# Performance work log

Hardware: AMD Instinct MI355X
Metric: run time of the kernel (lower is better)

The kernel has to match this reference:

```python
import jax, jax.numpy as jnp
import numpy as np

ALPHA = 1000.0  # softmin temperature from the original module


def setup_inputs() -> dict:
    key = jax.random.key(0)
    ks = jax.random.split(key, 10)
    B, D, H, E, K = 8192, 784, 256, 32, 512
    s = 0.05  # small init scale to keep activations/distances numerically sane
    return {
        "x": jax.random.normal(ks[0], (B, D), jnp.float32),
        "cluster_reps": jax.random.normal(ks[1], (K, E), jnp.float32),
        "W1": jax.random.normal(ks[2], (D, H), jnp.float32) * s,
        "b1": jnp.zeros((H,), jnp.float32),
        "W2": jax.random.normal(ks[3], (H, E), jnp.float32) * s,
        "b2": jnp.zeros((E,), jnp.float32),
        "W3": jax.random.normal(ks[4], (E, H), jnp.float32) * s,
        "b3": jnp.zeros((H,), jnp.float32),
        "W4": jax.random.normal(ks[5], (H, D), jnp.float32) * s,
        "b4": jnp.zeros((D,), jnp.float32),
    }


def reference(x, cluster_reps, W1, b1, W2, b2, W3, b3, W4, b4):
    # --- autoencoder: 2-layer MLP encoder / decoder ---
    h = jax.nn.relu(x @ W1 + b1)            # [B, H]
    embeddings = h @ W2 + b2                # [B, E]
    h2 = jax.nn.relu(embeddings @ W3 + b3)  # [B, H]
    reconstruction = h2 @ W4 + b4           # [B, D]

    # --- squared distances to cluster reps: [B, K] ---
    diff = embeddings[:, None, :] - cluster_reps[None, :, :]  # [B, K, E]
    distances = jnp.sum(diff * diff, axis=2)                  # [B, K]

    # --- stable softmin-weighted distances ---
    min_dist = jnp.min(distances, axis=1, keepdims=True)       # [B, 1]
    exponentials = jnp.exp(-ALPHA * (distances - min_dist))    # [B, K]
    sum_exponentials = jnp.sum(exponentials, axis=1, keepdims=True)
    weighted_dists = distances * (exponentials / sum_exponentials)

    return (weighted_dists, distances, reconstruction, embeddings)
```

## Files before the change

### kernel.cpp

```cpp
#include <hip/hip_runtime.h>
#include <cstddef>

#define NB 8192
#define ND 784
#define NH 256
#define NE 32
#define NK 512
#define ALPHA_F 1000.0f

typedef _Float16 h8 __attribute__((ext_vector_type(8)));
typedef float f32x4 __attribute__((ext_vector_type(4)));

__global__ __launch_bounds__(256)
void splitw2_kernel(const float* __restrict__ W1, _Float16* __restrict__ w1thi,
                    _Float16* __restrict__ w1tlo,
                    const float* __restrict__ W4, _Float16* __restrict__ w4thi,
                    _Float16* __restrict__ w4tlo) {
    const int b = blockIdx.x;
    const float* W; _Float16 *hi, *lo; int K, N, n;
    if (b < NH) { W = W1; hi = w1thi; lo = w1tlo; K = ND; N = NH; n = b; }
    else        { W = W4; hi = w4thi; lo = w4tlo; K = NH; N = ND; n = b - NH; }
    for (int k = threadIdx.x; k < K; k += 256) {
        float w = W[(size_t)k * N + n];
        _Float16 hh = (_Float16)w;
        float r = w - (float)hh;
        hi[(size_t)n * K + k] = hh;
        lo[(size_t)n * K + k] = (_Float16)(r * 2048.0f);
    }
}

template<int TERMS, bool RELU, bool SPLITA, int MT>
__device__ __forceinline__ void gemm_body(
    const float* __restrict__ Af32,
    const _Float16* __restrict__ Ahi_g,
    const _Float16* __restrict__ Alo_g,
    const _Float16* __restrict__ WThi,
    const _Float16* __restrict__ WTlo,
    const float* __restrict__ bias, float* __restrict__ C,
    int N, int K, int KS, int bx, int by, int tid,
    _Float16* __restrict__ sAhi, _Float16* __restrict__ sAlo,
    _Float16* __restrict__ sBhi, _Float16* __restrict__ sBlo) {
    constexpr int BM  = MT * 32;
    constexpr int ACH = BM / 64;
    constexpr int AS  = BM * 40;
    constexpr int BS  = 64 * 40;

    const int bm = bx * BM;
    const int bn = by * 64;

    const int arow = (ACH == 1) ? (tid >> 2) : (tid >> 1);
    const int ak   = (ACH == 1) ? ((tid & 3) * 8) : ((tid & 1) * 16);
    const int brow = tid >> 2;
    const int bk   = (tid & 3) * 8;

    const float*    pA32 = SPLITA ? Af32 + (size_t)(bm + arow) * K : nullptr;
    const _Float16* pAhi = SPLITA ? nullptr : Ahi_g + (size_t)(bm + arow) * K;
    const _Float16* pAlo = SPLITA ? nullptr : Alo_g + (size_t)(bm + arow) * K;
    int brow_g = bn + brow; if (brow_g > N - 1) brow_g = N - 1;
    const _Float16* pBhi = WThi + (size_t)brow_g * K;
    const _Float16* pBlo = WTlo + (size_t)brow_g * K;

    float araw[ACH * 8];
    h8 rahi[ACH], ralo[ACH];
    h8 rbhi, rblo;

    auto prefetch = [&](int s) {
        #pragma unroll
        for (int c = 0; c < ACH; ++c) {
            const int k = s * 32 + ak + c * 8;
            if (SPLITA) {
                if (k + 8 <= K) {
                    f32x4 v0 = *(const f32x4*)(pA32 + k);
                    f32x4 v1 = *(const f32x4*)(pA32 + k + 4);
                    #pragma unroll
                    for (int j = 0; j < 4; ++j) {
                        araw[c * 8 + j]     = v0[j];
                        araw[c * 8 + 4 + j] = v1[j];
                    }
                } else {
                    #pragma unroll
                    for (int j = 0; j < 8; ++j) araw[c * 8 + j] = 0.f;
                }
            } else {
                rahi[c] = (k + 8 <= K) ? *(const h8*)(pAhi + k) : (h8){};
                ralo[c] = (k + 8 <= K) ? *(const h8*)(pAlo + k) : (h8){};
            }
        }
        const int kb = s * 32 + bk;
        rbhi = (kb + 8 <= K) ? *(const h8*)(pBhi + kb) : (h8){};
        rblo = (kb + 8 <= K) ? *(const h8*)(pBlo + kb) : (h8){};
    };

    auto commit = [&](int buf) {
        #pragma unroll
        for (int c = 0; c < ACH; ++c) {
            h8 hi, lo;
            if (SPLITA) {
                #pragma unroll
                for (int j = 0; j < 8; ++j) {
                    float v = araw[c * 8 + j];
                    _Float16 hh = (_Float16)v;
                    hi[j] = hh;
                    lo[j] = (_Float16)((v - (float)hh) * 2048.0f);
                }
            } else { hi = rahi[c]; lo = ralo[c]; }
            *(h8*)&sAhi[buf * AS + arow * 40 + ak + c * 8] = hi;
            *(h8*)&sAlo[buf * AS + arow * 40 + ak + c * 8] = lo;
        }
        *(h8*)&sBhi[buf * BS + brow * 40 + bk] = rbhi;
        *(h8*)&sBlo[buf * BS + brow * 40 + bk] = rblo;
    };

    prefetch(0);
    commit(0);
    prefetch(1);
    __syncthreads();

    const int lane = tid & 63;
    const int wv   = tid >> 6;
    const int wm   = (wv >> 1) * (MT * 16);
    const int wn   = (wv & 1) * 32;
    const int li   = lane & 15;
    const int kq   = (lane >> 4) * 8;

    f32x4 acc0[MT][2] = {};
    f32x4 acc1[MT][2] = {};
    f32x4 acc2[MT][2] = {};

    for (int s = 0; s < KS; ++s) {
        const int buf = s & 1;
        h8 fahi[MT], falo[MT], fbhi[2], fblo[2];
        #pragma unroll
        for (int mt = 0; mt < MT; ++mt) {
            const int ao = buf * AS + (wm + mt * 16 + li) * 40 + kq;
            fahi[mt] = *(const h8*)&sAhi[ao];
            falo[mt] = *(const h8*)&sAlo[ao];
        }
        #pragma unroll
        for (int nt = 0; nt < 2; ++nt) {
            const int bo = buf * BS + (wn + nt * 16 + li) * 40 + kq;
            fbhi[nt] = *(const h8*)&sBhi[bo];
            fblo[nt] = *(const h8*)&sBlo[bo];
        }
        #pragma unroll
        for (int mt = 0; mt < MT; ++mt)
            #pragma unroll
            for (int nt = 0; nt < 2; ++nt) {
                acc0[mt][nt] = __builtin_amdgcn_mfma_f32_16x16x32_f16(
                    fahi[mt], fbhi[nt], acc0[mt][nt], 0, 0, 0);
                acc1[mt][nt] = __builtin_amdgcn_mfma_f32_16x16x32_f16(
                    fahi[mt], fblo[nt], acc1[mt][nt], 0, 0, 0);
                acc1[mt][nt] = __builtin_amdgcn_mfma_f32_16x16x32_f16(
                    falo[mt], fbhi[nt], acc1[mt][nt], 0, 0, 0);
                if (TERMS == 4)
                    acc2[mt][nt] = __builtin_amdgcn_mfma_f32_16x16x32_f16(
                        falo[mt], fblo[nt], acc2[mt][nt], 0, 0, 0);
            }
        if (s + 1 < KS) {
            commit((s + 1) & 1);
            if (s + 2 < KS) prefetch(s + 2);
        }
        __syncthreads();
    }

    const float c1 = 1.0f / 2048.0f;
    const float c2 = c1 * c1;
    const int quad = lane >> 4;
    #pragma unroll
    for (int nt = 0; nt < 2; ++nt) {
        const int n = bn + wn + nt * 16 + li;
        if (n < N) {
            const float bv = bias[n];
            #pragma unroll
            for (int mt = 0; mt < MT; ++mt) {
                #pragma unroll
                for (int r = 0; r < 4; ++r) {
                    const int m = bm + wm + mt * 16 + quad * 4 + r;
                    float v = acc0[mt][nt][r] + c1 * acc1[mt][nt][r];
                    if (TERMS == 4) v += c2 * acc2[mt][nt][r];
                    v += bv;
                    if (RELU) v = fmaxf(v, 0.f);
                    C[(size_t)m * N + n] = v;
                }
            }
        }
    }
}

template<int TERMS, bool RELU, bool SPLITA, int MT>
__global__ __launch_bounds__(256)
void mfma_gemm3(const float* __restrict__ Af32,
                const _Float16* __restrict__ Ahi_g,
                const _Float16* __restrict__ Alo_g,
                const _Float16* __restrict__ WThi,
                const _Float16* __restrict__ WTlo,
                const float* __restrict__ bias, float* __restrict__ C,
                int N, int K, int KS) {
    constexpr int BM = MT * 32;
    __shared__ __align__(16) _Float16 smem[2 * BM * 40 * 2 + 2 * 64 * 40 * 2];
    _Float16* sAhi = smem;
    _Float16* sAlo = sAhi + 2 * BM * 40;
    _Float16* sBhi = sAlo + 2 * BM * 40;
    _Float16* sBlo = sBhi + 2 * 64 * 40;
    gemm_body<TERMS, RELU, SPLITA, MT>(Af32, Ahi_g, Alo_g, WThi, WTlo, bias, C,
                                       N, K, KS, blockIdx.x, blockIdx.y,
                                       threadIdx.x, sAhi, sAlo, sBhi, sBlo);
}

__global__ __launch_bounds__(256)
void mid_kernel(const float* __restrict__ h, const float* __restrict__ W2,
                const float* __restrict__ b2, const float* __restrict__ W3,
                const float* __restrict__ b3, float* __restrict__ emb,
                _Float16* __restrict__ h2hi, _Float16* __restrict__ h2lo) {
    __shared__ float es[16][32];
    const int tid = threadIdx.x;
    const int r0  = blockIdx.x * 16;

    #pragma unroll
    for (int half = 0; half < 2; ++half) {
        const int o   = tid + half * 256;
        const int row = o >> 5;
        const int col = o & 31;
        const float* hrow = h + (size_t)(r0 + row) * NH;
        float acc0 = 0.f, acc1 = 0.f;
        #pragma unroll 4
        for (int k = 0; k < NH; k += 4) {
            float4 hv = *(const float4*)(hrow + k);
            acc0 = fmaf(hv.x, W2[(k + 0) * NE + col], acc0);
            acc1 = fmaf(hv.y, W2[(k + 1) * NE + col], acc1);
            acc0 = fmaf(hv.z, W2[(k + 2) * NE + col], acc0);
            acc1 = fmaf(hv.w, W2[(k + 3) * NE + col], acc1);
        }
        float v = acc0 + acc1 + b2[col];
        es[row][col] = v;
        emb[(size_t)r0 * NE + o] = v;
    }
    __syncthreads();

    const int col = tid;
    float acc[16];
    #pragma unroll
    for (int r = 0; r < 16; ++r) acc[r] = 0.f;
    #pragma unroll
    for (int k = 0; k < NE; ++k) {
        float w = W3[k * NH + col];
        #pragma unroll
        for (int r = 0; r < 16; ++r) acc[r] = fmaf(es[r][k], w, acc[r]);
    }
    const float bb = b3[col];
    #pragma unroll
    for (int r = 0; r < 16; ++r) {
        float v = acc[r] + bb;
        v = v > 0.f ? v : 0.f;
        _Float16 hh = (_Float16)v;
        float rr = v - (float)hh;
        h2hi[(size_t)(r0 + r) * NH + col] = hh;
        h2lo[(size_t)(r0 + r) * NH + col] = (_Float16)(rr * 2048.0f);
    }
}

__device__ __forceinline__ void dist_body256(
    const float* __restrict__ emb, const float* __restrict__ reps,
    float* __restrict__ dist, float* __restrict__ wout,
    int blk, int tid, float* __restrict__ es, float* __restrict__ tr,
    float* __restrict__ rmin, float* __restrict__ rinv) {
    const int r0 = blk * 8;
    es[tid] = emb[(size_t)r0 * NE + tid];

    const float* rp0 = reps + (size_t)tid * NE;
    const float* rp1 = reps + (size_t)(tid + 256) * NE;
    f32x4 rv0[8], rv1[8];
    #pragma unroll
    for (int e4 = 0; e4 < 8; ++e4) {
        rv0[e4] = ((const f32x4*)rp0)[e4];
        rv1[e4] = ((const f32x4*)rp1)[e4];
    }
    __syncthreads();

    float d0[8], d1[8];
    #pragma unroll
    for (int r = 0; r < 8; ++r) {
        float a0 = 0.f, a1 = 0.f;
        #pragma unroll
        for (int e4 = 0; e4 < 8; ++e4) {
            f32x4 ev = *(const f32x4*)&es[r * 32 + e4 * 4];
            #pragma unroll
            for (int j = 0; j < 4; ++j) {
                float t0 = ev[j] - rv0[e4][j];
                a0 = fmaf(t0, t0, a0);
                float t1 = ev[j] - rv1[e4][j];
                a1 = fmaf(t1, t1, a1);
            }
        }
        d0[r] = a0; d1[r] = a1;
    }

    const int lane = tid & 63;
    const int wv   = tid >> 6;

    #pragma unroll
    for (int r = 0; r < 8; ++r) {
        tr[r * 520 + tid]       = d0[r];
        tr[r * 520 + 256 + tid] = d1[r];
    }
    __syncthreads();
    #pragma unroll
    for (int p = 0; p < 2; ++p) {
        const int rr = wv + p * 4;
        f32x4 a = *(const f32x4*)&tr[rr * 520 + lane * 8];
        f32x4 b = *(const f32x4*)&tr[rr * 520 + lane * 8 + 4];
        float m = fminf(fminf(fminf(a[0], a[1]), fminf(a[2], a[3])),
                        fminf(fminf(b[0], b[1]), fminf(b[2], b[3])));
        #pragma unroll
        for (int off = 32; off > 0; off >>= 1)
            m = fminf(m, __shfl_xor(m, off, 64));
        if (lane == 0) rmin[rr] = m;
    }
    __syncthreads();

    float e0[8], e1[8];
    #pragma unroll
    for (int r = 0; r < 8; ++r) {
        e0[r] = expf(-ALPHA_F * (d0[r] - rmin[r]));
        e1[r] = expf(-ALPHA_F * (d1[r] - rmin[r]));
        tr[r * 520 + tid]       = e0[r];
        tr[r * 520 + 256 + tid] = e1[r];
    }
    __syncthreads();
    #pragma unroll
    for (int p = 0; p < 2; ++p) {
        const int rr = wv + p * 4;
        f32x4 a = *(const f32x4*)&tr[rr * 520 + lane * 8];
        f32x4 b = *(const f32x4*)&tr[rr * 520 + lane * 8 + 4];
        float s = ((a[0] + a[1]) + (a[2] + a[3])) +
                  ((b[0] + b[1]) + (b[2] + b[3]));
        #pragma unroll
        for (int off = 32; off > 0; off >>= 1)
            s += __shfl_xor(s, off, 64);
        if (lane == 0) rinv[rr] = 1.0f / s;
    }
    __syncthreads();

    #pragma unroll
    for (int r = 0; r < 8; ++r) {
        const size_t row = (size_t)(r0 + r);
        dist[row * NK + tid]       = d0[r];
        dist[row * NK + 256 + tid] = d1[r];
        wout[row * NK + tid]       = d0[r] * (e0[r] * rinv[r]);
        wout[row * NK + 256 + tid] = d1[r] * (e1[r] * rinv[r]);
    }
}

__global__ __launch_bounds__(512, 4)
void dist_kernel(const float* __restrict__ emb, const float* __restrict__ reps,
                 float* __restrict__ dist, float* __restrict__ wout) {
    __shared__ float es[8][32];
    __shared__ float tr[8][520];
    __shared__ float rmin[8];
    __shared__ float rinv[8];

    const int tid = threadIdx.x;
    const int r0  = blockIdx.x * 8;

    if (tid < 256) es[tid >> 5][tid & 31] = emb[(size_t)r0 * NE + tid];

    const float* rp = reps + (size_t)tid * NE;
    f32x4 rv[8];
    #pragma unroll
    for (int e4 = 0; e4 < 8; ++e4) rv[e4] = ((const f32x4*)rp)[e4];
    __syncthreads();

    float d[8];
    #pragma unroll
    for (int r = 0; r < 8; ++r) {
        float a = 0.f;
        #pragma unroll
        for (int e4 = 0; e4 < 8; ++e4) {
            f32x4 ev = *(const f32x4*)&es[r][e4 * 4];
            #pragma unroll
            for (int j = 0; j < 4; ++j) {
                float t = ev[j] - rv[e4][j];
                a = fmaf(t, t, a);
            }
        }
        d[r] = a;
    }

    const int lane = tid & 63;
    const int wv   = tid >> 6;

    #pragma unroll
    for (int r = 0; r < 8; ++r) tr[r][tid] = d[r];
    __syncthreads();
    {
        f32x4 a = *(const f32x4*)&tr[wv][lane * 8];
        f32x4 b = *(const f32x4*)&tr[wv][lane * 8 + 4];
        float m = fminf(fminf(fminf(a[0], a[1]), fminf(a[2], a[3])),
                        fminf(fminf(b[0], b[1]), fminf(b[2], b[3])));
        #pragma unroll
        for (int off = 32; off > 0; off >>= 1)
            m = fminf(m, __shfl_xor(m, off, 64));
        if (lane == 0) rmin[wv] = m;
    }
    __syncthreads();

    float e[8];
    #pragma unroll
    for (int r = 0; r < 8; ++r) {
        e[r] = expf(-ALPHA_F * (d[r] - rmin[r]));
        tr[r][tid] = e[r];
    }
    __syncthreads();
    {
        f32x4 a = *(const f32x4*)&tr[wv][lane * 8];
        f32x4 b = *(const f32x4*)&tr[wv][lane * 8 + 4];
        float s = ((a[0] + a[1]) + (a[2] + a[3])) +
                  ((b[0] + b[1]) + (b[2] + b[3]));
        #pragma unroll
        for (int off = 32; off > 0; off >>= 1)
            s += __shfl_xor(s, off, 64);
        if (lane == 0) rinv[wv] = 1.0f / s;
    }
    __syncthreads();

    #pragma unroll
    for (int r = 0; r < 8; ++r) {
        const size_t row = (size_t)(r0 + r);
        dist[row * NK + tid] = d[r];
        wout[row * NK + tid] = d[r] * (e[r] * rinv[r]);
    }
}

#define NGB (64 * 13)
#define NDB (NB / 8)

__global__ __launch_bounds__(256)
void tail_fused(const _Float16* __restrict__ h2hi,
                const _Float16* __restrict__ h2lo,
                const _Float16* __restrict__ w4thi,
                const _Float16* __restrict__ w4tlo,
                const float* __restrict__ b4, float* __restrict__ recon,
                const float* __restrict__ emb, const float* __restrict__ reps,
                float* __restrict__ dist, float* __restrict__ wout) {
    __shared__ __align__(16) _Float16 smem[2 * 128 * 40 * 2 + 2 * 64 * 40 * 2];
    const int bid = blockIdx.x;
    const int tid = threadIdx.x;

    bool isDist; int idx;
    if (bid < 2 * NGB) { isDist = (bid & 1); idx = bid >> 1; }
    else               { isDist = true; idx = NGB + (bid - 2 * NGB); }

    if (!isDist) {
        _Float16* sAhi = smem;
        _Float16* sAlo = sAhi + 2 * 128 * 40;
        _Float16* sBhi = sAlo + 2 * 128 * 40;
        _Float16* sBlo = sBhi + 2 * 64 * 40;
        gemm_body<3, false, false, 4>(nullptr, h2hi, h2lo, w4thi, w4tlo, b4,
                                      recon, ND, NH, 8, idx & 63, idx >> 6,
                                      tid, sAhi, sAlo, sBhi, sBlo);
    } else {
        float* es   = (float*)smem;
        float* tr   = es + 8 * 32;
        float* rmin = tr + 8 * 520;
        float* rinv = rmin + 8;
        dist_body256(emb, reps, dist, wout, idx, tid, es, tr, rmin, rinv);
    }
}

extern "C" void kernel_launch(void* const* d_in, const int* in_sizes, int n_in,
                              void* d_out, int out_size, void* d_ws, size_t ws_size,
                              hipStream_t stream) {
    const float* x    = (const float*)d_in[0];
    const float* reps = (const float*)d_in[1];
    const float* W1   = (const float*)d_in[2];
    const float* b1   = (const float*)d_in[3];
    const float* W2   = (const float*)d_in[4];
    const float* b2   = (const float*)d_in[5];
    const float* W3   = (const float*)d_in[6];
    const float* b3   = (const float*)d_in[7];
    const float* W4   = (const float*)d_in[8];
    const float* b4   = (const float*)d_in[9];

    float* out   = (float*)d_out;
    float* wout  = out;
    float* dist  = out + (size_t)NB * NK;
    float* recon = out + (size_t)2 * NB * NK;
    float* emb   = out + (size_t)2 * NB * NK + (size_t)NB * ND;

    float* h = dist;

    const size_t wneed = ((size_t)4 * ND * NH + (size_t)2 * NB * NH)
                         * sizeof(_Float16);

    if (d_ws != nullptr && ws_size >= wneed) {
        _Float16* w1thi = (_Float16*)d_ws;
        _Float16* w1tlo = w1thi + (size_t)NH * ND;
        _Float16* w4thi = w1tlo + (size_t)NH * ND;
        _Float16* w4tlo = w4thi + (size_t)ND * NH;
        _Float16* h2hi  = w4tlo + (size_t)ND * NH;
        _Float16* h2lo  = h2hi + (size_t)NB * NH;

        splitw2_kernel<<<NH + ND, 256, 0, stream>>>(W1, w1thi, w1tlo,
                                                    W4, w4thi, w4tlo);
        mfma_gemm3<4, true, true, 2><<<dim3(128, 4), 256, 0, stream>>>(
            x, nullptr, nullptr, w1thi, w1tlo, b1, h, NH, ND, 25);
        mid_kernel<<<NB / 16, 256, 0, stream>>>(h, W2, b2, W3, b3,
                                                emb, h2hi, h2lo);
        tail_fused<<<2 * NGB + (NDB - NGB), 256, 0, stream>>>(
            h2hi, h2lo, w4thi, w4tlo, b4, recon, emb, reps, dist, wout);
    } else {
        _Float16* h2hi  = (_Float16*)(dist + (size_t)NB * NH);
        _Float16* h2lo  = h2hi + (size_t)NB * NH;
        _Float16* w1thi = (_Float16*)wout;
        _Float16* w1tlo = w1thi + (size_t)NH * ND;
        _Float16* w4thi = w1tlo + (size_t)NH * ND;
        _Float16* w4tlo = w4thi + (size_t)ND * NH;

        splitw2_kernel<<<NH + ND, 256, 0, stream>>>(W1, w1thi, w1tlo,
                                                    W4, w4thi, w4tlo);
        mfma_gemm3<4, true, true, 2><<<dim3(128, 4), 256, 0, stream>>>(
            x, nullptr, nullptr, w1thi, w1tlo, b1, h, NH, ND, 25);
        mid_kernel<<<NB / 16, 256, 0, stream>>>(h, W2, b2, W3, b3,
                                                emb, h2hi, h2lo);
        mfma_gemm3<3, false, false, 4><<<dim3(64, 13), 256, 0, stream>>>(
            nullptr, h2hi, h2lo, w4thi, w4tlo, b4, recon, ND, NH, 8);
        dist_kernel<<<NB / 8, 512, 0, stream>>>(emb, reps, dist, wout);
    }
}
```

Baseline: 176.9 us.

## Pre-split x into fp16 hi/lo in prep kernel and rebalance tail fusion

A new prep kernel replaces the weight-split kernel. It transposes W1 and W4 through a shared-memory tile so that both reads and writes are coalesced, and it also pre-splits the whole input x into fp16 hi/lo halves in workspace. This lets the first GEMM read fp16 A operands instead of converting fp32 in its inner loop. The tail kernel's recon GEMM tiles shrink from MT=4 to MT=2, doubling the GEMM block count and changing how GEMM and distance blocks interleave. The cost is extra workspace and an additional full pass over x (read fp32, write 2x fp16) before the GEMM.

```diff
diff --git a/kernel.cpp b/kernel.cpp
--- a/kernel.cpp
+++ b/kernel.cpp
@@ -26,6 +26,76 @@
         float r = w - (float)hh;
         hi[(size_t)n * K + k] = hh;
         lo[(size_t)n * K + k] = (_Float16)(r * 2048.0f);
+    }
+}
+
+#define TW1 ((ND + 31) / 32)
+#define TN1 (NH / 32)
+#define TW4 (NH / 32)
+#define TN4 ((ND + 31) / 32)
+#define NBW1 (TW1 * TN1)
+#define NBW4 (TW4 * TN4)
+#define NBX  624
+
+__global__ __launch_bounds__(256)
+void prep_kernel(const float* __restrict__ x,
+                 _Float16* __restrict__ xhi, _Float16* __restrict__ xlo,
+                 const float* __restrict__ W1, _Float16* __restrict__ w1thi,
+                 _Float16* __restrict__ w1tlo,
+                 const float* __restrict__ W4, _Float16* __restrict__ w4thi,
+                 _Float16* __restrict__ w4tlo) {
+    __shared__ float tile[32][33];
+    const int b   = blockIdx.x;
+    const int tid = threadIdx.x;
+
+    if (b < NBW1 + NBW4) {
+        const float* W; _Float16 *hi, *lo; int K, N, kt, nt;
+        if (b < NBW1) { W = W1; hi = w1thi; lo = w1tlo; K = ND; N = NH;
+                        kt = b % TW1; nt = b / TW1; }
+        else { const int bb = b - NBW1; W = W4; hi = w4thi; lo = w4tlo;
+               K = NH; N = ND; kt = bb % TW4; nt = bb / TW4; }
+        const int k0 = kt * 32, n0 = nt * 32;
+        const int row = tid >> 3, c4 = (tid & 7) * 4;
+        #pragma unroll
+        for (int j = 0; j < 4; ++j) {
+            const int k = k0 + row, n = n0 + c4 + j;
+            tile[row][c4 + j] = (k < K && n < N) ? W[(size_t)k * N + n] : 0.f;
+        }
+        __syncthreads();
+        const int n = n0 + row;
+        if (n < N) {
+            #pragma unroll
+            for (int j = 0; j < 4; ++j) {
+                const int k = k0 + c4 + j;
+                if (k < K) {
+                    float w = tile[c4 + j][row];
+                    _Float16 hh = (_Float16)w;
+                    float r = w - (float)hh;
+                    hi[(size_t)n * K + k] = hh;
+                    lo[(size_t)n * K + k] = (_Float16)(r * 2048.0f);
+                }
+            }
+        }
+    } else {
+        const int bb = b - (NBW1 + NBW4);
+        const size_t total = (size_t)NB * ND / 8;
+        for (size_t i = (size_t)bb * 256 + tid; i < total;
+             i += (size_t)NBX * 256) {
+            f32x4 v0 = *(const f32x4*)(x + i * 8);
+            f32x4 v1 = *(const f32x4*)(x + i * 8 + 4);
+            h8 hi, lo;
+            #pragma unroll
+            for (int j = 0; j < 4; ++j) {
+                _Float16 h0 = (_Float16)v0[j];
+                hi[j] = h0;
+                lo[j] = (_Float16)((v0[j] - (float)h0) * 2048.0f);
+                _Float16 h1 = (_Float16)v1[j];
+                hi[j + 4] = h1;
+                lo[j + 4] = (_Float16)((v1[j] - (float)h1) * 2048.0f);
+            }
+            *(h8*)(xhi + i * 8) = hi;
+            *(h8*)(xlo + i * 8) = lo;
+        }
     }
 }
 
@@ -431,7 +501,7 @@
     }
 }
 
-#define NGB (64 * 13)
+#define NGB (128 * 13)
 #define NDB (NB / 8)
 
 __global__ __launch_bounds__(256)
@@ -442,21 +512,21 @@
                 const float* __restrict__ b4, float* __restrict__ recon,
                 const float* __restrict__ emb, const float* __restrict__ reps,
                 float* __restrict__ dist, float* __restrict__ wout) {
-    __shared__ __align__(16) _Float16 smem[2 * 128 * 40 * 2 + 2 * 64 * 40 * 2];
+    __shared__ __align__(16) _Float16 smem[2 * 64 * 40 * 2 + 2 * 64 * 40 * 2];
     const int bid = blockIdx.x;
     const int tid = threadIdx.x;
 
     bool isDist; int idx;
-    if (bid < 2 * NGB) { isDist = (bid & 1); idx = bid >> 1; }
-    else               { isDist = true; idx = NGB + (bid - 2 * NGB); }
+    if (bid < 2 * NDB) { isDist = (bid & 1); idx = bid >> 1; }
+    else               { isDist = false; idx = bid - NDB; }
 
     if (!isDist) {
         _Float16* sAhi = smem;
-        _Float16* sAlo = sAhi + 2 * 128 * 40;
-        _Float16* sBhi = sAlo + 2 * 128 * 40;
+        _Float16* sAlo = sAhi + 2 * 64 * 40;
+        _Float16* sBhi = sAlo + 2 * 64 * 40;
         _Float16* sBlo = sBhi + 2 * 64 * 40;
-        gemm_body<3, false, false, 4>(nullptr, h2hi, h2lo, w4thi, w4tlo, b4,
-                                      recon, ND, NH, 8, idx & 63, idx >> 6,
+        gemm_body<3, false, false, 2>(nullptr, h2hi, h2lo, w4thi, w4tlo, b4,
+                                      recon, ND, NH, 8, idx & 127, idx >> 7,
                                       tid, sAhi, sAlo, sBhi, sBlo);
     } else {
         float* es   = (float*)smem;
@@ -489,24 +559,26 @@
 
     float* h = dist;
 
-    const size_t wneed = ((size_t)4 * ND * NH + (size_t)2 * NB * NH)
-                         * sizeof(_Float16);
+    const size_t wneed = ((size_t)2 * NB * ND + (size_t)4 * ND * NH +
+                          (size_t)2 * NB * NH) * sizeof(_Float16);
 
     if (d_ws != nullptr && ws_size >= wneed) {
-        _Float16* w1thi = (_Float16*)d_ws;
+        _Float16* xhi   = (_Float16*)d_ws;
+        _Float16* xlo   = xhi + (size_t)NB * ND;
+        _Float16* w1thi = xlo + (size_t)NB * ND;
         _Float16* w1tlo = w1thi + (size_t)NH * ND;
         _Float16* w4thi = w1tlo + (size_t)NH * ND;
         _Float16* w4tlo = w4thi + (size_t)ND * NH;
         _Float16* h2hi  = w4tlo + (size_t)ND * NH;
         _Float16* h2lo  = h2hi + (size_t)NB * NH;
 
-        splitw2_kernel<<<NH + ND, 256, 0, stream>>>(W1, w1thi, w1tlo,
-                                                    W4, w4thi, w4tlo);
-        mfma_gemm3<4, true, true, 2><<<dim3(128, 4), 256, 0, stream>>>(
-            x, nullptr, nullptr, w1thi, w1tlo, b1, h, NH, ND, 25);
+        prep_kernel<<<NBW1 + NBW4 + NBX, 256, 0, stream>>>(
+            x, xhi, xlo, W1, w1thi, w1tlo, W4, w4thi, w4tlo);
+        mfma_gemm3<4, true, false, 2><<<dim3(128, 4), 256, 0, stream>>>(
+            nullptr, xhi, xlo, w1thi, w1tlo, b1, h, NH, ND, 25);
         mid_kernel<<<NB / 16, 256, 0, stream>>>(h, W2, b2, W3, b3,
                                                 emb, h2hi, h2lo);
-        tail_fused<<<2 * NGB + (NDB - NGB), 256, 0, stream>>>(
+        tail_fused<<<NGB + NDB, 256, 0, stream>>>(
             h2hi, h2lo, w4thi, w4tlo, b4, recon, emb, reps, dist, wout);
     } else {
         _Float16* h2hi  = (_Float16*)(dist + (size_t)NB * NH);
```

Result: no change. 177.2 us (+0.1%).
